# Kernel tuning notes

Measured on AMD Instinct MI355X. Metric: run time of the kernel, lower is better.

Reference implementation:

```python
import jax, jax.numpy as jnp
import numpy as np

NH = 8  # num_heads


def _conv1x1(w, b, x):
    # 1x1 conv == channel matmul: w [O,C], x [B,C,H,W]
    return jnp.einsum('oc,bchw->bohw', w, x) + b[None, :, None, None]


def _fwd(low_freq_feat, high_freq_feat, ext_context, road_feat,
         ext_proj_w, ext_proj_b, road_proj_w, road_proj_b,
         ext_qkv_w, ext_qkv_b, road_qkv_w, road_qkv_b,
         ext_out_w, ext_out_b, road_out_w, road_out_b,
         gate_ext_w, gate_ext_b, gate_road_w, gate_road_b):
    B, C, H, W = low_freq_feat.shape
    nh = NH
    hd = C // nh
    HW = H * W
    scale = hd ** -0.5

    ext_p = ext_context @ ext_proj_w.T + ext_proj_b          # [B,C]
    road_p = _conv1x1(road_proj_w, road_proj_b, road_feat)   # [B,C,H,W]

    eqkv = (ext_p @ ext_qkv_w.T + ext_qkv_b).reshape(B, 3, nh, hd)
    ext_q, ext_v = eqkv[:, 0], eqkv[:, 2]                    # [B,nh,hd]

    # torch: conv out [B,3C,H,W] viewed as (B,C,3,H,W) -> q/k/v interleaved over channels
    rqkv = _conv1x1(road_qkv_w, road_qkv_b, road_p).reshape(B, C, 3, H, W)
    road_k = rqkv[:, :, 1].reshape(B, nh, hd, HW).transpose(0, 1, 3, 2)  # [B,nh,HW,hd]
    road_v = rqkv[:, :, 2].reshape(B, nh, hd, HW).transpose(0, 1, 3, 2)

    # ext->road attention. The torch code expands ext_q to HW identical rows; one row
    # per (batch, head) gives a bit-identical result without the [B,nh,HW,HW] blowup.
    scores = jnp.einsum('bnd,bnpd->bnp', ext_q, road_k) * scale
    attn = jax.nn.softmax(scores, axis=-1)                   # [B,nh,HW]
    ext_head = jnp.einsum('bnp,bnpd->bnd', attn, road_v).reshape(B, C)
    ext_vec = ext_head @ ext_out_w.T + ext_out_b             # [B,C]
    ext_feat_spatial = jnp.broadcast_to(ext_vec[:, :, None, None], (B, C, H, W))

    # road->ext attention: all HW keys/values are copies of the single ext token, so
    # softmax is exactly uniform and the output per position is exactly ext_v. The
    # road_out 1x1 conv on a spatially-constant map is a single matvec per batch.
    road_vec = ext_v.reshape(B, C) @ road_out_w.T + road_out_b
    road_enhanced = jnp.broadcast_to(road_vec[:, :, None, None], (B, C, H, W))

    # gated fusion (ext stream): spatial mean of constant map == ext_vec
    gate_in = jnp.concatenate([low_freq_feat.mean(axis=(2, 3)), ext_vec], axis=-1)
    ext_gate = jax.nn.sigmoid(gate_in @ gate_ext_w.T + gate_ext_b)[:, :, None, None]
    ext_final = low_freq_feat * (1.0 - ext_gate) + ext_feat_spatial * ext_gate

    # gated fusion (road stream)
    rg_in = jnp.concatenate([high_freq_feat, road_enhanced], axis=1)  # [B,2C,H,W]
    road_gate = jax.nn.sigmoid(_conv1x1(gate_road_w, gate_road_b, rg_in))
    road_final = high_freq_feat * (1.0 - road_gate) + road_enhanced * road_gate
    return ext_final, road_final


def setup_inputs() -> dict:
    key = jax.random.key(0)
    ks = jax.random.split(key, 20)
    B, C, H, W, E = 8, 256, 64, 64, 64
    f = lambda k, shape, s=1.0: jax.random.normal(k, shape, dtype=jnp.float32) * s
    return {
        'low_freq_feat': f(ks[0], (B, C, H, W)),
        'high_freq_feat': f(ks[1], (B, C, H, W)),
        'ext_context': f(ks[2], (B, E)),
        'road_feat': f(ks[3], (B, C, H, W)),
        'ext_proj_w': f(ks[4], (C, E), 0.05), 'ext_proj_b': f(ks[5], (C,), 0.02),
        'road_proj_w': f(ks[6], (C, C), 0.05), 'road_proj_b': f(ks[7], (C,), 0.02),
        'ext_qkv_w': f(ks[8], (3 * C, C), 0.05), 'ext_qkv_b': f(ks[9], (3 * C,), 0.02),
        'road_qkv_w': f(ks[10], (3 * C, C), 0.05), 'road_qkv_b': f(ks[11], (3 * C,), 0.02),
        'ext_out_w': f(ks[12], (C, C), 0.05), 'ext_out_b': f(ks[13], (C,), 0.02),
        'road_out_w': f(ks[14], (C, C), 0.05), 'road_out_b': f(ks[15], (C,), 0.02),
        'gate_ext_w': f(ks[16], (C, 2 * C), 0.05), 'gate_ext_b': f(ks[17], (C,), 0.02),
        'gate_road_w': f(ks[18], (C, 2 * C), 0.05), 'gate_road_b': f(ks[19], (C,), 0.02),
    }


def reference(low_freq_feat, high_freq_feat, ext_context, road_feat,
              ext_proj_w, ext_proj_b, road_proj_w, road_proj_b,
              ext_qkv_w, ext_qkv_b, road_qkv_w, road_qkv_b,
              ext_out_w, ext_out_b, road_out_w, road_out_b,
              gate_ext_w, gate_ext_b, gate_road_w, gate_road_b):
    return _fwd(low_freq_feat, high_freq_feat, ext_context, road_feat,
                ext_proj_w, ext_proj_b, road_proj_w, road_proj_b,
                ext_qkv_w, ext_qkv_b, road_qkv_w, road_qkv_b,
                ext_out_w, ext_out_b, road_out_w, road_out_b,
                gate_ext_w, gate_ext_b, gate_road_w, gate_road_b)
```

## Files before the change

### kernel.cpp

```cpp
#include <hip/hip_runtime.h>

typedef short bf16x8 __attribute__((ext_vector_type(8)));
typedef float f32x4 __attribute__((ext_vector_type(4)));

__device__ __forceinline__ unsigned short f2b(float f) {
    unsigned int u = __builtin_bit_cast(unsigned int, f);
    unsigned int r = u + 0x7FFFu + ((u >> 16) & 1u);
    return (unsigned short)(r >> 16);
}
__device__ __forceinline__ float wsum64(float v) {
    #pragma unroll
    for (int m = 32; m; m >>= 1) v += __shfl_xor(v, m, 64);
    return v;
}

__global__ __launch_bounds__(256) void k_setup(const float* __restrict__ w1,
                                               const float* __restrict__ wqkv,
                                               const float* __restrict__ b1,
                                               const float* __restrict__ bqkv,
                                               const float* __restrict__ gate_road_w,
                                               const float* __restrict__ ext_proj_w,
                                               const float* __restrict__ ext_qkv_w,
                                               const float* __restrict__ road_out_w,
                                               const float* __restrict__ low,
                                               unsigned short* __restrict__ W3b,
                                               unsigned short* __restrict__ Wcb,
                                               unsigned short* __restrict__ WF,
                                               float* __restrict__ bcv,
                                               float* __restrict__ mean_low) {
    int bid = blockIdx.x, t = threadIdx.x;
    __shared__ float sel[8][256];
    __shared__ float red[8][4];
    if (bid >= 400) {
        int bc = bid - 400;
        const f32x4* p4 = (const f32x4*)(low + (size_t)bc * 4096);
        float s = 0.f;
        for (int i = t; i < 1024; i += 256) {
            f32x4 v = p4[i];
            s += v[0] + v[1] + v[2] + v[3];
        }
        s = wsum64(s);
        if ((t & 63) == 0) red[0][t >> 6] = s;
        __syncthreads();
        if (t == 0) mean_low[bc] = (red[0][0] + red[0][1] + red[0][2] + red[0][3]) * (1.0f / 4096.0f);
    } else if (bid < 256) {
        int i = bid * 256 + t;
        int o = i >> 8, k = i & 255;
        W3b[i] = f2b(gate_road_w[o * 512 + k]);
    } else if (bid < 320) {
        int o0 = (bid - 256) * 8;
        #pragma unroll
        for (int r = 0; r < 8; r++) {
            int o = o0 + r;
            int c = (o < 256) ? o : o - 256;
            int g = (o < 256) ? 1 : 2;
            sel[r][t] = wqkv[(size_t)(3 * c + g) * 256 + t];
        }
        __syncthreads();
        float b1v = b1[t];
        #pragma unroll
        for (int r = 0; r < 8; r++) {
            float v = wsum64(sel[r][t] * b1v);
            if ((t & 63) == 0) red[r][t >> 6] = v;
        }
        __syncthreads();
        if (t < 8) {
            int o = o0 + t;
            int c = (o < 256) ? o : o - 256;
            int g = (o < 256) ? 1 : 2;
            bcv[o] = red[t][0] + red[t][1] + red[t][2] + red[t][3] + bqkv[3 * c + g];
        }
        float acc[8] = {};
        #pragma unroll 16
        for (int m = 0; m < 256; m++) {
            float w1v = w1[(size_t)m * 256 + t];
            #pragma unroll
            for (int r = 0; r < 8; r++) acc[r] += sel[r][m] * w1v;
        }
        #pragma unroll
        for (int r = 0; r < 8; r++) Wcb[(size_t)(o0 + r) * 256 + t] = f2b(acc[r]);
    } else {
        int mb = bid - 320;
        int m = mb >> 4, ctile = mb & 15;
        const float* src;
        int stride, K, coff;
        unsigned short* dst;
        if (m == 0)      { src = ext_qkv_w;                     stride = 256; K = 256; coff = 0;   dst = WF; }
        else if (m == 1) { src = ext_qkv_w + (size_t)512 * 256; stride = 256; K = 256; coff = 0;   dst = WF + 65536; }
        else if (m == 2) { src = road_out_w;                    stride = 256; K = 256; coff = 0;   dst = WF + 131072; }
        else if (m == 3) { src = gate_road_w;                   stride = 512; K = 256; coff = 256; dst = WF + 196608; }
        else             { src = ext_proj_w;                    stride = 64;  K = 64;  coff = 0;   dst = WF + 262144; }
        int lc = t >> 4, kseg = t & 15;
        int k0 = kseg * 16;
        if (k0 < K) {
            int c = ctile * 16 + lc;
            const float* sp = src + (size_t)c * stride + coff + k0;
            f32x4 v0 = *(const f32x4*)sp;
            f32x4 v1 = *(const f32x4*)(sp + 4);
            f32x4 v2 = *(const f32x4*)(sp + 8);
            f32x4 v3 = *(const f32x4*)(sp + 12);
            int kk = kseg >> 1;
            int Kt = K >> 5;
            #pragma unroll
            for (int h = 0; h < 2; h++) {
                int lhi = (kseg & 1) * 2 + h;
                int lane = lhi * 16 + lc;
                bf16x8 o;
                f32x4 a = h ? v2 : v0, b = h ? v3 : v1;
                #pragma unroll
                for (int i = 0; i < 4; i++) { o[i] = (short)f2b(a[i]); o[4 + i] = (short)f2b(b[i]); }
                *(bf16x8*)(dst + ((size_t)(ctile * Kt + kk) << 9) + lane * 8) = o;
            }
        }
    }
}

__global__ __launch_bounds__(256) void k_tiny(const unsigned short* __restrict__ WF,
                                              const float* __restrict__ ext_context,
                                              const float* __restrict__ ext_proj_b,
                                              const float* __restrict__ ext_qkv_b,
                                              const float* __restrict__ road_out_b,
                                              const float* __restrict__ gate_road_b,
                                              float* __restrict__ ext_q,
                                              float* __restrict__ road_vec,
                                              float* __restrict__ rg_const) {
    __shared__ unsigned short xA[16][264];
    __shared__ unsigned short xB[16][264];
    int t = threadIdx.x;
    int w = t >> 6, lane = t & 63, l15 = lane & 15, lhi = lane >> 4;
    const unsigned short* WqF  = WF;
    const unsigned short* WvF  = WF + 65536;
    const unsigned short* WroF = WF + 131072;
    const unsigned short* WgF  = WF + 196608;
    const unsigned short* WpF  = WF + 262144;
    for (int i = t; i < 8 * 132; i += 256) {
        int r = 8 + i / 132, cc = (i % 132) * 2;
        *(unsigned int*)&xA[r][cc] = 0;
        *(unsigned int*)&xB[r][cc] = 0;
    }
    {
        int b = t >> 5, k0 = (t & 31) * 2;
        float c0v = ext_context[b * 64 + k0];
        float c1v = ext_context[b * 64 + k0 + 1];
        *(unsigned int*)&xA[b][k0] = (unsigned int)f2b(c0v) | ((unsigned int)f2b(c1v) << 16);
    }
    __syncthreads();
    {
        f32x4 acc[4] = {};
        #pragma unroll
        for (int kk = 0; kk < 2; kk++) {
            bf16x8 a = *(const bf16x8*)&xA[l15][kk * 32 + 8 * lhi];
            #pragma unroll
            for (int ni = 0; ni < 4; ni++) {
                int ct = w * 4 + ni;
                bf16x8 bfr = *(const bf16x8*)(WpF + ((size_t)(ct * 2 + kk) << 9) + lane * 8);
                acc[ni] = __builtin_amdgcn_mfma_f32_16x16x32_bf16(a, bfr, acc[ni], 0, 0, 0);
            }
        }
        if (lhi < 2) {
            #pragma unroll
            for (int ni = 0; ni < 4; ni++) {
                int c = w * 64 + ni * 16 + l15;
                float bp = ext_proj_b[c];
                #pragma unroll
                for (int r = 0; r < 4; r++)
                    xB[4 * lhi + r][c] = f2b(acc[ni][r] + bp);
            }
        }
    }
    __syncthreads();
    {
        f32x4 acc[8] = {};
        bool isq = (w < 2);
        int cbase = (w & 1) * 128;
        const unsigned short* Wb = isq ? WqF : WvF;
        for (int kk = 0; kk < 8; kk++) {
            bf16x8 a = *(const bf16x8*)&xB[l15][kk * 32 + 8 * lhi];
            #pragma unroll
            for (int ni = 0; ni < 8; ni++) {
                int ct = (cbase >> 4) + ni;
                bf16x8 bfr = *(const bf16x8*)(Wb + ((size_t)(ct * 8 + kk) << 9) + lane * 8);
                acc[ni] = __builtin_amdgcn_mfma_f32_16x16x32_bf16(a, bfr, acc[ni], 0, 0, 0);
            }
        }
        if (lhi < 2) {
            #pragma unroll
            for (int ni = 0; ni < 8; ni++) {
                int c = cbase + ni * 16 + l15;
                float bb = ext_qkv_b[(isq ? 0 : 512) + c];
                #pragma unroll
                for (int r = 0; r < 4; r++) {
                    int b = 4 * lhi + r;
                    float val = acc[ni][r] + bb;
                    if (isq) ext_q[b * 256 + c] = val;
                    else     xA[b][c] = f2b(val);
                }
            }
        }
    }
    __syncthreads();
    {
        f32x4 acc[4] = {};
        for (int kk = 0; kk < 8; kk++) {
            bf16x8 a = *(const bf16x8*)&xA[l15][kk * 32 + 8 * lhi];
            #pragma unroll
            for (int ni = 0; ni < 4; ni++) {
                int ct = w * 4 + ni;
                bf16x8 bfr = *(const bf16x8*)(WroF + ((size_t)(ct * 8 + kk) << 9) + lane * 8);
                acc[ni] = __builtin_amdgcn_mfma_f32_16x16x32_bf16(a, bfr, acc[ni], 0, 0, 0);
            }
        }
        if (lhi < 2) {
            #pragma unroll
            for (int ni = 0; ni < 4; ni++) {
                int c = w * 64 + ni * 16 + l15;
                float bb = road_out_b[c];
                #pragma unroll
                for (int r = 0; r < 4; r++) {
                    int b = 4 * lhi + r;
                    float val = acc[ni][r] + bb;
                    road_vec[b * 256 + c] = val;
                    xB[b][c] = f2b(val);
                }
            }
        }
    }
    __syncthreads();
    {
        f32x4 acc[4] = {};
        for (int kk = 0; kk < 8; kk++) {
            bf16x8 a = *(const bf16x8*)&xB[l15][kk * 32 + 8 * lhi];
            #pragma unroll
            for (int ni = 0; ni < 4; ni++) {
                int ct = w * 4 + ni;
                bf16x8 bfr = *(const bf16x8*)(WgF + ((size_t)(ct * 8 + kk) << 9) + lane * 8);
                acc[ni] = __builtin_amdgcn_mfma_f32_16x16x32_bf16(a, bfr, acc[ni], 0, 0, 0);
            }
        }
        if (lhi < 2) {
            #pragma unroll
            for (int ni = 0; ni < 4; ni++) {
                int c = w * 64 + ni * 16 + l15;
                float bb = gate_road_b[c];
                #pragma unroll
                for (int r = 0; r < 4; r++)
                    rg_const[(4 * lhi + r) * 256 + c] = acc[ni][r] + bb;
            }
        }
    }
}

__global__ __launch_bounds__(512) void k_main(const float* __restrict__ road_feat,
                                              const float* __restrict__ high,
                                              const unsigned short* __restrict__ Wcb,
                                              const unsigned short* __restrict__ W3b,
                                              const float* __restrict__ bcv,
                                              const float* __restrict__ extq,
                                              const float* __restrict__ rg_const,
                                              const float* __restrict__ road_vec,
                                              float* __restrict__ part,
                                              float* __restrict__ outbuf) {
    __shared__ __align__(16) char smem[33792];
    int bid = blockIdx.x;
    int role = bid & 1, tile = bid >> 1;
    int b  = tile >> 7;
    int p0 = (tile & 127) << 5;
    int t  = threadIdx.x;
    int w = t >> 6, lane = t & 63, l15 = lane & 15, lhi = lane >> 4;

    if (role == 0) {
        char* Xc = smem;
        float (*esh)[32] = (float (*)[32])(smem + 16384);
        const float* rfb = road_feat + (size_t)b * 1048576;
        int c0 = 2 * (t >> 3);
        int j4 = (t & 7) * 4;
        #pragma unroll
        for (int it = 0; it < 2; ++it) {
            int c = c0 + 128 * it;
            f32x4 g0 = *(const f32x4*)(rfb + (size_t)c * 4096 + p0 + j4);
            f32x4 g1 = *(const f32x4*)(rfb + (size_t)(c + 1) * 4096 + p0 + j4);
            #pragma unroll
            for (int i = 0; i < 4; i++) {
                int j = j4 + i;
                unsigned int pk = (unsigned int)f2b(g0[i]) | ((unsigned int)f2b(g1[i]) << 16);
                *(unsigned int*)(Xc + ((j * 512 + 2 * c) ^ ((j & 15) << 4))) = pk;
            }
        }
        __syncthreads();

        f32x4 acc[2][4] = {};
        #pragma unroll
        for (int ni = 0; ni < 4; ni++) {
            const unsigned short* wrow = Wcb + (size_t)(w * 64 + ni * 16 + l15) * 256 + 8 * lhi;
            bf16x8 wf[8];
            #pragma unroll
            for (int kk = 0; kk < 8; kk++) wf[kk] = *(const bf16x8*)(wrow + kk * 32);
            #pragma unroll
            for (int kk = 0; kk < 8; kk++) {
                int base = (kk * 32 + 8 * lhi) * 2;
                bf16x8 a0 = *(const bf16x8*)(Xc + ((l15 * 512 + base) ^ (l15 << 4)));
                bf16x8 a1 = *(const bf16x8*)(Xc + (((16 + l15) * 512 + base) ^ (l15 << 4)));
                acc[0][ni] = __builtin_amdgcn_mfma_f32_16x16x32_bf16(a0, wf[kk], acc[0][ni], 0, 0, 0);
                acc[1][ni] = __builtin_amdgcn_mfma_f32_16x16x32_bf16(a1, wf[kk], acc[1][ni], 0, 0, 0);
            }
        }

        if (w < 4) {
            float qv[4], bk[4];
            #pragma unroll
            for (int ni = 0; ni < 4; ni++) {
                int n = w * 64 + ni * 16 + l15;
                qv[ni] = extq[b * 256 + n];
                bk[ni] = bcv[n];
            }
            #pragma unroll
            for (int mi = 0; mi < 2; mi++)
                #pragma unroll
                for (int r = 0; r < 4; r++) {
                    int j = mi * 16 + 4 * lhi + r;
                    #pragma unroll
                    for (int hl = 0; hl < 2; hl++) {
                        float s = (acc[mi][2 * hl][r] + bk[2 * hl]) * qv[2 * hl]
                                + (acc[mi][2 * hl + 1][r] + bk[2 * hl + 1]) * qv[2 * hl + 1];
                        s += __shfl_xor(s, 1, 64);
                        s += __shfl_xor(s, 2, 64);
                        s += __shfl_xor(s, 4, 64);
                        s += __shfl_xor(s, 8, 64);
                        if (l15 == 0)
                            esh[w * 2 + hl][j] = expf(s * 0.17677669529663687f);
                    }
                }
        }
        __syncthreads();

        float* pb = part + (size_t)tile * 264;
        if (w >= 4) {
            #pragma unroll
            for (int ni = 0; ni < 4; ni++) {
                int cv = (w - 4) * 64 + ni * 16 + l15;
                int hg = (w - 4) * 2 + (ni >> 1);
                float bv = bcv[256 + cv];
                float p = 0.f;
                #pragma unroll
                for (int mi = 0; mi < 2; mi++)
                    #pragma unroll
                    for (int r = 0; r < 4; r++) {
                        int j = mi * 16 + 4 * lhi + r;
                        p += esh[hg][j] * (acc[mi][ni][r] + bv);
                    }
                p += __shfl_xor(p, 16, 64);
                p += __shfl_xor(p, 32, 64);
                if (lhi == 0) pb[8 + cv] = p;
            }
        } else {
            int h0 = w * 2;
            float v0 = (lane < 32) ? esh[h0][lane] : esh[h0 + 1][lane - 32];
            v0 += __shfl_xor(v0, 1, 64);
            v0 += __shfl_xor(v0, 2, 64);
            v0 += __shfl_xor(v0, 4, 64);
            v0 += __shfl_xor(v0, 8, 64);
            v0 += __shfl_xor(v0, 16, 64);
            if (lane == 0)  pb[h0] = v0;
            if (lane == 32) pb[h0 + 1] = v0;
        }
    } else {
        char* Xc = smem;
        const float* hb = high + (size_t)b * 1048576;
        int c0 = t >> 3;
        int j4 = (t & 7) * 4;
        #pragma unroll
        for (int it = 0; it < 4; ++it) {
            int c = c0 + 64 * it;
            f32x4 g = *(const f32x4*)(hb + (size_t)c * 4096 + p0 + j4);
            #pragma unroll
            for (int i = 0; i < 4; i++) {
                int j = j4 + i;
                *(float*)(Xc + ((j * 1024 + 4 * c) ^ ((j & 15) << 4))) = g[i];
            }
        }
        __syncthreads();

        f32x4 acc[2][2] = {};
        #pragma unroll
        for (int ni = 0; ni < 2; ni++) {
            const unsigned short* wrow = W3b + (size_t)(w * 32 + ni * 16 + l15) * 256 + 8 * lhi;
            bf16x8 wf[8];
            #pragma unroll
            for (int kk = 0; kk < 8; kk++) wf[kk] = *(const bf16x8*)(wrow + kk * 32);
            #pragma unroll
            for (int kk = 0; kk < 8; kk++) {
                int base = (kk * 32 + 8 * lhi) * 4;
                int sw0 = l15 << 4;
                f32x4 x0 = *(const f32x4*)(Xc + ((l15 * 1024 + base) ^ sw0));
                f32x4 x1 = *(const f32x4*)(Xc + ((l15 * 1024 + base + 16) ^ sw0));
                f32x4 y0 = *(const f32x4*)(Xc + (((16 + l15) * 1024 + base) ^ sw0));
                f32x4 y1 = *(const f32x4*)(Xc + (((16 + l15) * 1024 + base + 16) ^ sw0));
                bf16x8 a0, a1;
                #pragma unroll
                for (int i = 0; i < 4; i++) {
                    a0[i] = (short)f2b(x0[i]); a0[4 + i] = (short)f2b(x1[i]);
                    a1[i] = (short)f2b(y0[i]); a1[4 + i] = (short)f2b(y1[i]);
                }
                acc[0][ni] = __builtin_amdgcn_mfma_f32_16x16x32_bf16(a0, wf[kk], acc[0][ni], 0, 0, 0);
                acc[1][ni] = __builtin_amdgcn_mfma_f32_16x16x32_bf16(a1, wf[kk], acc[1][ni], 0, 0, 0);
            }
        }
        __syncthreads();

        #pragma unroll
        for (int ni = 0; ni < 2; ni++) {
            int o = w * 32 + ni * 16 + l15;
            float rc = rg_const[b * 256 + o];
            float rv = road_vec[b * 256 + o];
            #pragma unroll
            for (int mi = 0; mi < 2; mi++)
                #pragma unroll
                for (int r = 0; r < 4; r++) {
                    int j = mi * 16 + 4 * lhi + r;
                    float* slot = (float*)(Xc + ((j * 1024 + 4 * o) ^ ((j & 15) << 4)));
                    float z = acc[mi][ni][r] + rc;
                    float gte = 1.0f / (1.0f + expf(-z));
                    float hv = *slot;
                    *slot = hv + gte * (rv - hv);
                }
        }
        __syncthreads();

        float* ob = outbuf + 8388608 + (size_t)b * 1048576;
        #pragma unroll
        for (int it = 0; it < 4; ++it) {
            int c = c0 + 64 * it;
            f32x4 o4;
            #pragma unroll
            for (int i = 0; i < 4; i++) {
                int j = j4 + i;
                o4[i] = *(const float*)(Xc + ((j * 1024 + 4 * c) ^ ((j & 15) << 4)));
            }
            *(f32x4*)(ob + (size_t)c * 4096 + p0 + j4) = o4;
        }
    }
}

__global__ __launch_bounds__(256) void k_vec(const float* __restrict__ part,
                                             const float* __restrict__ ext_out_w,
                                             const float* __restrict__ ext_out_b,
                                             const float* __restrict__ mean_low,
                                             const float* __restrict__ gate_ext_w,
                                             const float* __restrict__ gate_ext_b,
                                             float* __restrict__ ext_vec,
                                             float* __restrict__ ext_gate) {
    int b = blockIdx.x, c = threadIdx.x;
    __shared__ float hd_[256], ev[256], ml[256], tot[8];
    const float* pb = part + (size_t)b * 128 * 264;
    float a = 0.f;
    #pragma unroll 4
    for (int tile = 0; tile < 128; tile++) a += pb[tile * 264 + 8 + c];
    if (c < 8) {
        float s = 0.f;
        for (int tile = 0; tile < 128; tile++) s += pb[tile * 264 + c];
        tot[c] = 1.0f / s;
    }
    ml[c] = mean_low[b * 256 + c];
    __syncthreads();
    hd_[c] = a * tot[c >> 5];
    __syncthreads();
    float s = ext_out_b[c];
    #pragma unroll 4
    for (int k = 0; k < 256; k++) s += ext_out_w[c * 256 + k] * hd_[k];
    ext_vec[b * 256 + c] = s;
    ev[c] = s;
    __syncthreads();
    float z = gate_ext_b[c];
    #pragma unroll 4
    for (int k = 0; k < 256; k++)
        z += gate_ext_w[c * 512 + k] * ml[k] + gate_ext_w[c * 512 + 256 + k] * ev[k];
    ext_gate[b * 256 + c] = 1.0f / (1.0f + expf(-z));
}

__global__ __launch_bounds__(256) void k_ext_final(const float* __restrict__ low,
                                                   const float* __restrict__ ext_vec,
                                                   const float* __restrict__ ext_gate,
                                                   float* __restrict__ out) {
    int idx = blockIdx.x * 256 + threadIdx.x;
    #pragma unroll
    for (int rep = 0; rep < 4; ++rep) {
        int i = idx + rep * 524288;
        int bc = i >> 10;
        float g = ext_gate[bc];
        float vv = ext_vec[bc];
        f32x4 L = *(const f32x4*)(low + (size_t)i * 4);
        f32x4 o;
        #pragma unroll
        for (int c = 0; c < 4; c++) o[c] = L[c] + g * (vv - L[c]);
        *(f32x4*)(out + (size_t)i * 4) = o;
    }
}

extern "C" void kernel_launch(void* const* d_in, const int* in_sizes, int n_in,
                              void* d_out, int out_size, void* d_ws, size_t ws_size,
                              hipStream_t stream) {
    const float* low         = (const float*)d_in[0];
    const float* high        = (const float*)d_in[1];
    const float* ext_context = (const float*)d_in[2];
    const float* road_feat   = (const float*)d_in[3];
    const float* ext_proj_w  = (const float*)d_in[4];
    const float* ext_proj_b  = (const float*)d_in[5];
    const float* road_proj_w = (const float*)d_in[6];
    const float* road_proj_b = (const float*)d_in[7];
    const float* ext_qkv_w   = (const float*)d_in[8];
    const float* ext_qkv_b   = (const float*)d_in[9];
    const float* road_qkv_w  = (const float*)d_in[10];
    const float* road_qkv_b  = (const float*)d_in[11];
    const float* ext_out_w   = (const float*)d_in[12];
    const float* ext_out_b   = (const float*)d_in[13];
    const float* road_out_w  = (const float*)d_in[14];
    const float* road_out_b  = (const float*)d_in[15];
    const float* gate_ext_w  = (const float*)d_in[16];
    const float* gate_ext_b  = (const float*)d_in[17];
    const float* gate_road_w = (const float*)d_in[18];
    const float* gate_road_b = (const float*)d_in[19];

    float* out = (float*)d_out;
    unsigned short* wsb = (unsigned short*)d_ws;
    unsigned short* Wcb = wsb;
    unsigned short* W3b = wsb + 131072;
    unsigned short* WF  = wsb + 196608;
    float* fw = (float*)((char*)d_ws + 983040);
    float* ext_q    = fw;
    float* road_vec = fw + 2048;
    float* rg_const = fw + 4096;
    float* ext_vec  = fw + 8192;
    float* ext_gate = fw + 10240;
    float* mean_low = fw + 12288;
    float* bcv      = fw + 14336;
    float* part = out + 2097152;

    k_setup<<<2448, 256, 0, stream>>>(road_proj_w, road_qkv_w, road_proj_b, road_qkv_b,
                                      gate_road_w, ext_proj_w, ext_qkv_w, road_out_w, low,
                                      W3b, Wcb, WF, bcv, mean_low);
    k_tiny<<<1, 256, 0, stream>>>(WF, ext_context, ext_proj_b, ext_qkv_b,
                                  road_out_b, gate_road_b, ext_q, road_vec, rg_const);
    k_main<<<2048, 512, 0, stream>>>(road_feat, high, Wcb, W3b, bcv, ext_q,
                                     rg_const, road_vec, part, out);
    k_vec<<<8, 256, 0, stream>>>(part, ext_out_w, ext_out_b, mean_low,
                                 gate_ext_w, gate_ext_b, ext_vec, ext_gate);
    k_ext_final<<<2048, 256, 0, stream>>>(low, ext_vec, ext_gate, out);
}
```

Measured before the change: 182.1 us.

## Split main kernel into KV and road kernels with double-buffered two-tile pipelining

```diff
diff --git a/kernel.cpp b/kernel.cpp
--- a/kernel.cpp
+++ b/kernel.cpp
@@ -250,61 +250,53 @@
     }
 }
 
-__global__ __launch_bounds__(512) void k_main(const float* __restrict__ road_feat,
-                                              const float* __restrict__ high,
-                                              const unsigned short* __restrict__ Wcb,
-                                              const unsigned short* __restrict__ W3b,
-                                              const float* __restrict__ bcv,
-                                              const float* __restrict__ extq,
-                                              const float* __restrict__ rg_const,
-                                              const float* __restrict__ road_vec,
-                                              float* __restrict__ part,
-                                              float* __restrict__ outbuf) {
-    __shared__ __align__(16) char smem[33792];
-    int bid = blockIdx.x;
-    int role = bid & 1, tile = bid >> 1;
-    int b  = tile >> 7;
-    int p0 = (tile & 127) << 5;
-    int t  = threadIdx.x;
+__global__ __launch_bounds__(512) void k_kv(const float* __restrict__ road_feat,
+                                            const unsigned short* __restrict__ Wcb,
+                                            const float* __restrict__ bcv,
+                                            const float* __restrict__ extq,
+                                            float* __restrict__ part) {
+    __shared__ unsigned short Xs[2][32 * 256];
+    __shared__ float esh[2][8][32];
+    int t = threadIdx.x;
     int w = t >> 6, lane = t & 63, l15 = lane & 15, lhi = lane >> 4;
-
-    if (role == 0) {
-        char* Xc = smem;
-        float (*esh)[32] = (float (*)[32])(smem + 16384);
-        const float* rfb = road_feat + (size_t)b * 1048576;
-        int c0 = 2 * (t >> 3);
-        int j4 = (t & 7) * 4;
-        #pragma unroll
-        for (int it = 0; it < 2; ++it) {
-            int c = c0 + 128 * it;
-            f32x4 g0 = *(const f32x4*)(rfb + (size_t)c * 4096 + p0 + j4);
-            f32x4 g1 = *(const f32x4*)(rfb + (size_t)(c + 1) * 4096 + p0 + j4);
-            #pragma unroll
-            for (int i = 0; i < 4; i++) {
-                int j = j4 + i;
-                unsigned int pk = (unsigned int)f2b(g0[i]) | ((unsigned int)f2b(g1[i]) << 16);
-                *(unsigned int*)(Xc + ((j * 512 + 2 * c) ^ ((j & 15) << 4))) = pk;
-            }
-        }
-        __syncthreads();
-
+    int c0 = 2 * (t >> 3);
+    int j4 = (t & 7) * 4;
+    f32x4 g0, g1, g2, g3;
+
+    auto LOAD = [&](int tl) {
+        const float* rfb = road_feat + (size_t)(tl >> 7) * 1048576 + ((tl & 127) << 5);
+        g0 = *(const f32x4*)(rfb + (size_t)c0 * 4096 + j4);
+        g1 = *(const f32x4*)(rfb + (size_t)(c0 + 1) * 4096 + j4);
+        g2 = *(const f32x4*)(rfb + (size_t)(c0 + 128) * 4096 + j4);
+        g3 = *(const f32x4*)(rfb + (size_t)(c0 + 129) * 4096 + j4);
+    };
+    auto WRITE = [&](int buf) {
+        char* Xc = (char*)Xs[buf];
+        #pragma unroll
+        for (int i = 0; i < 4; i++) {
+            int j = j4 + i;
+            int sw = (j & 15) << 4;
+            unsigned int pkA = (unsigned int)f2b(g0[i]) | ((unsigned int)f2b(g1[i]) << 16);
+            unsigned int pkB = (unsigned int)f2b(g2[i]) | ((unsigned int)f2b(g3[i]) << 16);
+            *(unsigned int*)(Xc + ((j * 512 + 2 * c0) ^ sw)) = pkA;
+            *(unsigned int*)(Xc + ((j * 512 + 2 * (c0 + 128)) ^ sw)) = pkB;
+        }
+    };
+    auto COMPUTE = [&](int buf, int tl) {
+        char* Xc = (char*)Xs[buf];
+        int b = tl >> 7;
         f32x4 acc[2][4] = {};
-        #pragma unroll
-        for (int ni = 0; ni < 4; ni++) {
-            const unsigned short* wrow = Wcb + (size_t)(w * 64 + ni * 16 + l15) * 256 + 8 * lhi;
-            bf16x8 wf[8];
-            #pragma unroll
-            for (int kk = 0; kk < 8; kk++) wf[kk] = *(const bf16x8*)(wrow + kk * 32);
-            #pragma unroll
-            for (int kk = 0; kk < 8; kk++) {
-                int base = (kk * 32 + 8 * lhi) * 2;
-                bf16x8 a0 = *(const bf16x8*)(Xc + ((l15 * 512 + base) ^ (l15 << 4)));
-                bf16x8 a1 = *(const bf16x8*)(Xc + (((16 + l15) * 512 + base) ^ (l15 << 4)));
-                acc[0][ni] = __builtin_amdgcn_mfma_f32_16x16x32_bf16(a0, wf[kk], acc[0][ni], 0, 0, 0);
-                acc[1][ni] = __builtin_amdgcn_mfma_f32_16x16x32_bf16(a1, wf[kk], acc[1][ni], 0, 0, 0);
-            }
-        }
-
+        for (int kk = 0; kk < 8; kk++) {
+            int base = (kk * 32 + 8 * lhi) * 2;
+            bf16x8 a0 = *(const bf16x8*)(Xc + ((l15 * 512 + base) ^ (l15 << 4)));
+            bf16x8 a1 = *(const bf16x8*)(Xc + (((16 + l15) * 512 + base) ^ (l15 << 4)));
+            #pragma unroll
+            for (int ni = 0; ni < 4; ni++) {
+                bf16x8 wfr = *(const bf16x8*)(Wcb + (size_t)(w * 64 + ni * 16 + l15) * 256 + kk * 32 + 8 * lhi);
+                acc[0][ni] = __builtin_amdgcn_mfma_f32_16x16x32_bf16(a0, wfr, acc[0][ni], 0, 0, 0);
+                acc[1][ni] = __builtin_amdgcn_mfma_f32_16x16x32_bf16(a1, wfr, acc[1][ni], 0, 0, 0);
+            }
+        }
         if (w < 4) {
             float qv[4], bk[4];
             #pragma unroll
@@ -327,13 +319,12 @@
                         s += __shfl_xor(s, 4, 64);
                         s += __shfl_xor(s, 8, 64);
                         if (l15 == 0)
-                            esh[w * 2 + hl][j] = expf(s * 0.17677669529663687f);
+                            esh[buf][w * 2 + hl][j] = expf(s * 0.17677669529663687f);
                     }
                 }
         }
         __syncthreads();
-
-        float* pb = part + (size_t)tile * 264;
+        float* pb = part + (size_t)tl * 264;
         if (w >= 4) {
             #pragma unroll
             for (int ni = 0; ni < 4; ni++) {
@@ -346,7 +337,7 @@
                     #pragma unroll
                     for (int r = 0; r < 4; r++) {
                         int j = mi * 16 + 4 * lhi + r;
-                        p += esh[hg][j] * (acc[mi][ni][r] + bv);
+                        p += esh[buf][hg][j] * (acc[mi][ni][r] + bv);
                     }
                 p += __shfl_xor(p, 16, 64);
                 p += __shfl_xor(p, 32, 64);
@@ -354,7 +345,7 @@
             }
         } else {
             int h0 = w * 2;
-            float v0 = (lane < 32) ? esh[h0][lane] : esh[h0 + 1][lane - 32];
+            float v0 = (lane < 32) ? esh[buf][h0][lane] : esh[buf][h0 + 1][lane - 32];
             v0 += __shfl_xor(v0, 1, 64);
             v0 += __shfl_xor(v0, 2, 64);
             v0 += __shfl_xor(v0, 4, 64);
@@ -363,50 +354,81 @@
             if (lane == 0)  pb[h0] = v0;
             if (lane == 32) pb[h0 + 1] = v0;
         }
-    } else {
-        char* Xc = smem;
-        const float* hb = high + (size_t)b * 1048576;
-        int c0 = t >> 3;
-        int j4 = (t & 7) * 4;
-        #pragma unroll
-        for (int it = 0; it < 4; ++it) {
-            int c = c0 + 64 * it;
-            f32x4 g = *(const f32x4*)(hb + (size_t)c * 4096 + p0 + j4);
+    };
+
+    int t0 = blockIdx.x, t1 = blockIdx.x + 512;
+    LOAD(t0);
+    WRITE(0);
+    __syncthreads();
+    LOAD(t1);
+    COMPUTE(0, t0);
+    WRITE(1);
+    __syncthreads();
+    COMPUTE(1, t1);
+}
+
+__global__ __launch_bounds__(512) void k_road(const float* __restrict__ high,
+                                              const unsigned short* __restrict__ W3b,
+                                              const float* __restrict__ rg_const,
+                                              const float* __restrict__ road_vec,
+                                              float* __restrict__ outbuf) {
+    __shared__ float Xs[2][32 * 256];
+    int t = threadIdx.x;
+    int w = t >> 6, lane = t & 63, l15 = lane & 15, lhi = lane >> 4;
+    int c0 = t >> 3;
+    int j4 = (t & 7) * 4;
+    f32x4 g0, g1, g2, g3;
+
+    auto LOAD = [&](int tl) {
+        const float* hb = high + (size_t)(tl >> 7) * 1048576 + ((tl & 127) << 5);
+        g0 = *(const f32x4*)(hb + (size_t)c0 * 4096 + j4);
+        g1 = *(const f32x4*)(hb + (size_t)(c0 + 64) * 4096 + j4);
+        g2 = *(const f32x4*)(hb + (size_t)(c0 + 128) * 4096 + j4);
+        g3 = *(const f32x4*)(hb + (size_t)(c0 + 192) * 4096 + j4);
+    };
+    auto WRITE = [&](int buf) {
+        char* Xc = (char*)Xs[buf];
+        #pragma unroll
+        for (int i = 0; i < 4; i++) {
+            int j = j4 + i;
+            int sw = (j & 15) << 4;
+            *(float*)(Xc + ((j * 1024 + 4 * c0) ^ sw))         = g0[i];
+            *(float*)(Xc + ((j * 1024 + 4 * (c0 + 64)) ^ sw))  = g1[i];
+            *(float*)(Xc + ((j * 1024 + 4 * (c0 + 128)) ^ sw)) = g2[i];
+            *(float*)(Xc + ((j * 1024 + 4 * (c0 + 192)) ^ sw)) = g3[i];
+        }
+    };
+
+    int tl0 = blockIdx.x, tl1 = blockIdx.x + 512;
+    f32x4 acc[2][2];
+
+    auto GEMM = [&](int buf) {
+        char* Xc = (char*)Xs[buf];
+        acc[0][0] = f32x4{}; acc[0][1] = f32x4{};
+        acc[1][0] = f32x4{}; acc[1][1] = f32x4{};
+        for (int kk = 0; kk < 8; kk++) {
+            int base = (kk * 32 + 8 * lhi) * 4;
+            int sw0 = l15 << 4;
+            f32x4 x0 = *(const f32x4*)(Xc + ((l15 * 1024 + base) ^ sw0));
+            f32x4 x1 = *(const f32x4*)(Xc + ((l15 * 1024 + base + 16) ^ sw0));
+            f32x4 y0 = *(const f32x4*)(Xc + (((16 + l15) * 1024 + base) ^ sw0));
+            f32x4 y1 = *(const f32x4*)(Xc + (((16 + l15) * 1024 + base + 16) ^ sw0));
+            bf16x8 a0, a1;
             #pragma unroll
             for (int i = 0; i < 4; i++) {
-                int j = j4 + i;
-                *(float*)(Xc + ((j * 1024 + 4 * c) ^ ((j & 15) << 4))) = g[i];
-            }
-        }
-        __syncthreads();
-
-        f32x4 acc[2][2] = {};
-        #pragma unroll
-        for (int ni = 0; ni < 2; ni++) {
-            const unsigned short* wrow = W3b + (size_t)(w * 32 + ni * 16 + l15) * 256 + 8 * lhi;
-            bf16x8 wf[8];
-            #pragma unroll
-            for (int kk = 0; kk < 8; kk++) wf[kk] = *(const bf16x8*)(wrow + kk * 32);
-            #pragma unroll
-            for (int kk = 0; kk < 8; kk++) {
-                int base = (kk * 32 + 8 * lhi) * 4;
-                int sw0 = l15 << 4;
-                f32x4 x0 = *(const f32x4*)(Xc + ((l15 * 1024 + base) ^ sw0));
-                f32x4 x1 = *(const f32x4*)(Xc + ((l15 * 1024 + base + 16) ^ sw0));
-                f32x4 y0 = *(const f32x4*)(Xc + (((16 + l15) * 1024 + base) ^ sw0));
-                f32x4 y1 = *(const f32x4*)(Xc + (((16 + l15) * 1024 + base + 16) ^ sw0));
-                bf16x8 a0, a1;
-                #pragma unroll
-                for (int i = 0; i < 4; i++) {
-                    a0[i] = (short)f2b(x0[i]); a0[4 + i] = (short)f2b(x1[i]);
-                    a1[i] = (short)f2b(y0[i]); a1[4 + i] = (short)f2b(y1[i]);
-                }
-                acc[0][ni] = __builtin_amdgcn_mfma_f32_16x16x32_bf16(a0, wf[kk], acc[0][ni], 0, 0, 0);
-                acc[1][ni] = __builtin_amdgcn_mfma_f32_16x16x32_bf16(a1, wf[kk], acc[1][ni], 0, 0, 0);
-            }
-        }
-        __syncthreads();
-
+                a0[i] = (short)f2b(x0[i]); a0[4 + i] = (short)f2b(x1[i]);
+                a1[i] = (short)f2b(y0[i]); a1[4 + i] = (short)f2b(y1[i]);
+            }
+            #pragma unroll
+            for (int ni = 0; ni < 2; ni++) {
+                bf16x8 wfr = *(const bf16x8*)(W3b + (size_t)(w * 32 + ni * 16 + l15) * 256 + kk * 32 + 8 * lhi);
+                acc[0][ni] = __builtin_amdgcn_mfma_f32_16x16x32_bf16(a0, wfr, acc[0][ni], 0, 0, 0);
+                acc[1][ni] = __builtin_amdgcn_mfma_f32_16x16x32_bf16(a1, wfr, acc[1][ni], 0, 0, 0);
+            }
+        }
+    };
+    auto GATE = [&](int buf, int b) {
+        char* Xc = (char*)Xs[buf];
         #pragma unroll
         for (int ni = 0; ni < 2; ni++) {
             int o = w * 32 + ni * 16 + l15;
@@ -424,9 +446,10 @@
                     *slot = hv + gte * (rv - hv);
                 }
         }
-        __syncthreads();
-
-        float* ob = outbuf + 8388608 + (size_t)b * 1048576;
+    };
+    auto STREAMOUT = [&](int buf, int tl) {
+        char* Xc = (char*)Xs[buf];
+        float* ob = outbuf + 8388608 + (size_t)(tl >> 7) * 1048576 + ((tl & 127) << 5);
         #pragma unroll
         for (int it = 0; it < 4; ++it) {
             int c = c0 + 64 * it;
@@ -436,9 +459,25 @@
                 int j = j4 + i;
                 o4[i] = *(const float*)(Xc + ((j * 1024 + 4 * c) ^ ((j & 15) << 4)));
             }
-            *(f32x4*)(ob + (size_t)c * 4096 + p0 + j4) = o4;
-        }
-    }
+            *(f32x4*)(ob + (size_t)c * 4096 + j4) = o4;
+        }
+    };
+
+    LOAD(tl0);
+    WRITE(0);
+    __syncthreads();
+    LOAD(tl1);
+    GEMM(0);
+    __syncthreads();
+    WRITE(1);
+    GATE(0, tl0 >> 7);
+    __syncthreads();
+    STREAMOUT(0, tl0);
+    GEMM(1);
+    __syncthreads();
+    GATE(1, tl1 >> 7);
+    __syncthreads();
+    STREAMOUT(1, tl1);
 }
 
 __global__ __launch_bounds__(256) void k_vec(const float* __restrict__ part,
@@ -540,8 +579,8 @@
                                       W3b, Wcb, WF, bcv, mean_low);
     k_tiny<<<1, 256, 0, stream>>>(WF, ext_context, ext_proj_b, ext_qkv_b,
                                   road_out_b, gate_road_b, ext_q, road_vec, rg_const);
-    k_main<<<2048, 512, 0, stream>>>(road_feat, high, Wcb, W3b, bcv, ext_q,
-                                     rg_const, road_vec, part, out);
+    k_kv<<<512, 512, 0, stream>>>(road_feat, Wcb, bcv, ext_q, part);
+    k_road<<<512, 512, 0, stream>>>(high, W3b, rg_const, road_vec, out);
     k_vec<<<8, 256, 0, stream>>>(part, ext_out_w, ext_out_b, mean_low,
                                  gate_ext_w, gate_ext_b, ext_vec, ext_gate);
     k_ext_final<<<2048, 256, 0, stream>>>(low, ext_vec, ext_gate, out);
```

Result: slower. 188.8 us (+3.7%).
